# Optimization experiments

Measured on AMD Instinct MI355X. Metric: run time of the kernel, lower is better.

The kernel has to match this reference:

```python
import jax, jax.numpy as jnp
import numpy as np

G, NPG, HID, NLAYERS, MAXZ, K = 256, 128, 256, 3, 1000, 30
N = G * NPG          # 32768 nodes
E = N * 16           # 524288 edges
TOTAL_DIM = HID * NLAYERS + 1  # 769


def setup_inputs():
    key = jax.random.key(0)
    ks = jax.random.split(key, 12)
    z = jax.random.randint(ks[0], (N,), 0, MAXZ)
    edge_index = jax.random.randint(ks[1], (2, E), 0, N)
    batch = jnp.arange(N) // NPG  # contiguous equal-size graphs
    emb = jax.random.normal(ks[2], (MAXZ, HID), jnp.float32)
    s = 1.0 / np.sqrt(HID)
    gcn_w = jax.random.normal(ks[3], (NLAYERS, HID, HID), jnp.float32) * s
    gcn_b = jnp.zeros((NLAYERS, HID), jnp.float32)
    gcn_w_last = jax.random.normal(ks[4], (HID, 1), jnp.float32) * s
    gcn_b_last = jnp.zeros((1,), jnp.float32)
    conv1_w = jax.random.normal(ks[5], (16, 1, 5), jnp.float32) * (1.0 / np.sqrt(5))
    conv1_b = jnp.zeros((16,), jnp.float32)
    conv2_w = jax.random.normal(ks[6], (32, 16, 5), jnp.float32) * (1.0 / np.sqrt(80))
    conv2_b = jnp.zeros((32,), jnp.float32)
    kd = K * TOTAL_DIM            # 23070
    flat = 32 * ((kd - 4) // 2 - 4)  # 368928
    lin1_w = jax.random.normal(ks[7], (128, flat), jnp.float32) * (1.0 / np.sqrt(flat))
    lin1_b = jnp.zeros((128,), jnp.float32)
    lin2_w = jax.random.normal(ks[8], (1, 128), jnp.float32) * (1.0 / np.sqrt(128))
    lin2_b = jnp.zeros((1,), jnp.float32)
    return dict(z=z, edge_index=edge_index, batch=batch, emb=emb, gcn_w=gcn_w,
                gcn_b=gcn_b, gcn_w_last=gcn_w_last, gcn_b_last=gcn_b_last,
                conv1_w=conv1_w, conv1_b=conv1_b, conv2_w=conv2_w, conv2_b=conv2_b,
                lin1_w=lin1_w, lin1_b=lin1_b, lin2_w=lin2_w, lin2_b=lin2_b)


def reference(z, edge_index, batch, emb, gcn_w, gcn_b, gcn_w_last, gcn_b_last,
              conv1_w, conv1_b, conv2_w, conv2_b, lin1_w, lin1_b, lin2_w, lin2_b):
    src, dst = edge_index[0], edge_index[1]
    # GCNConv normalization with self-loops: D^{-1/2}(A+I)D^{-1/2}
    deg = 1.0 + jax.ops.segment_sum(jnp.ones((E,), jnp.float32), dst, num_segments=N)
    dinv = jax.lax.rsqrt(deg)
    enorm = dinv[src] * dinv[dst]   # per-edge norm
    snorm = 1.0 / deg               # self-loop norm

    def gcn(x, W, b):
        xw = x @ W
        agg = jax.ops.segment_sum(enorm[:, None] * xw[src], dst, num_segments=N)
        return agg + snorm[:, None] * xw + b

    x = emb[z]
    xs = []
    for i in range(NLAYERS):
        x = jnp.tanh(gcn(x, gcn_w[i], gcn_b[i]))
        xs.append(x)
    xs.append(jnp.tanh(gcn(x, gcn_w_last, gcn_b_last)))
    h = jnp.concatenate(xs, axis=-1)  # [N, TOTAL_DIM]

    # global_sort_pool: per-graph descending sort by last channel, keep top-k
    hg = h.reshape(G, NPG, TOTAL_DIM)
    order = jnp.argsort(-hg[:, :, -1], axis=1)
    hg = jnp.take_along_axis(hg, order[:, :, None], axis=1)[:, :K]
    p = hg.reshape(G, 1, K * TOTAL_DIM)

    dn = ('NCH', 'OIH', 'NCH')
    c = jax.lax.conv_general_dilated(p, conv1_w, (1,), 'VALID', dimension_numbers=dn)
    c = jax.nn.relu(c + conv1_b[None, :, None])
    c = jax.lax.reduce_window(c, -jnp.inf, jax.lax.max, (1, 1, 2), (1, 1, 2), 'VALID')
    c = jax.lax.conv_general_dilated(c, conv2_w, (1,), 'VALID', dimension_numbers=dn)
    c = jax.nn.relu(c + conv2_b[None, :, None])
    f = c.reshape(G, -1)
    f = jax.nn.relu(f @ lin1_w.T + lin1_b)
    return (f @ lin2_w.T + lin2_b).reshape(-1)
```

## Files before the change

kernel.cpp:

```cpp
#include <hip/hip_runtime.h>

#define NN      32768
#define EE      524288
#define GG      256
#define NPG     128
#define HID     256
#define KTOP    30
#define TD      769
#define HSTR    772
#define PLEN    23070
#define C1LEN   23066
#define POOLLEN 11533
#define C2LEN   11529
#define FLAT    368928
#define L1_KRANGE 512
#define L1_KS   721

#define SWZ(c) ((c) + 4 * ((c) >> 5))

__global__ __launch_bounds__(256) void k_deg(const int* __restrict__ dst, int* __restrict__ deg_cnt) {
    int e = blockIdx.x * 256 + threadIdx.x;
    atomicAdd(&deg_cnt[dst[e]], 1);
}

__global__ __launch_bounds__(256) void k_norm(const int* __restrict__ deg_cnt,
                                              float* __restrict__ dinv, float* __restrict__ snorm) {
    int n = blockIdx.x * 256 + threadIdx.x;
    float dg = 1.0f + (float)deg_cnt[n];
    dinv[n] = rsqrtf(dg);
    snorm[n] = 1.0f / dg;
}

__global__ __launch_bounds__(1024) void k_scan(const int* __restrict__ deg_cnt, int* __restrict__ row_start) {
    __shared__ int sA[1024];
    int t = threadIdx.x;
    int base = t * 32;
    int s = 0;
    for (int i = 0; i < 32; i++) s += deg_cnt[base + i];
    sA[t] = s;
    __syncthreads();
    for (int off = 1; off < 1024; off <<= 1) {
        int v = (t >= off) ? sA[t - off] : 0;
        __syncthreads();
        sA[t] += v;
        __syncthreads();
    }
    int run = sA[t] - s;
    for (int i = 0; i < 32; i++) { row_start[base + i] = run; run += deg_cnt[base + i]; }
}

__global__ __launch_bounds__(256) void k_csrfill(const int* __restrict__ src, const int* __restrict__ dst,
                                                 const int* __restrict__ row_start, int* __restrict__ fill,
                                                 const float* __restrict__ dinv,
                                                 int* __restrict__ csr_src, float* __restrict__ csr_w) {
    int e = blockIdx.x * 256 + threadIdx.x;
    int s = src[e], d = dst[e];
    int pos = row_start[d] + atomicAdd(&fill[d], 1);
    csr_src[pos] = s;
    csr_w[pos] = dinv[s] * dinv[d];
}

__global__ __launch_bounds__(256) void k_embed(const int* __restrict__ z, const float* __restrict__ emb,
                                               float* __restrict__ x) {
    int i = blockIdx.x * 256 + threadIdx.x;
    int n = i >> 6, l = i & 63;
    ((float4*)x)[(size_t)n * 64 + l] = ((const float4*)emb)[(size_t)z[n] * 64 + l];
}

__global__ __launch_bounds__(256) void k_gemm_gcn(const float* __restrict__ A, const float* __restrict__ B,
                                                  float* __restrict__ C) {
    __shared__ float As[16][132];
    __shared__ float Bs[16][140];
    int m0 = blockIdx.x * 128;
    int n0 = blockIdx.y * 128;
    int tid = threadIdx.x;
    int ty = tid >> 4, tx = tid & 15;
    float acc[8][8] = {};
    for (int k0 = 0; k0 < 256; k0 += 16) {
        {
            int m = tid >> 2, kq = (tid & 3) * 4;
            #pragma unroll
            for (int r = 0; r < 2; r++) {
                float4 v = *(const float4*)&A[(size_t)(m0 + m + 64 * r) * 256 + k0 + kq];
                As[kq + 0][m + 64 * r] = v.x;
                As[kq + 1][m + 64 * r] = v.y;
                As[kq + 2][m + 64 * r] = v.z;
                As[kq + 3][m + 64 * r] = v.w;
            }
            int n = (tid & 31) * 4, kk = tid >> 5;
            #pragma unroll
            for (int r = 0; r < 2; r++) {
                float4 v = *(const float4*)&B[(size_t)(k0 + kk + 8 * r) * 256 + n0 + n];
                *(float4*)&Bs[kk + 8 * r][SWZ(n)] = v;
            }
        }
        __syncthreads();
        #pragma unroll
        for (int k = 0; k < 16; k++) {
            float a[8], b[8];
            *(float4*)&a[0] = *(float4*)&As[k][ty * 8];
            *(float4*)&a[4] = *(float4*)&As[k][ty * 8 + 4];
            *(float4*)&b[0] = *(float4*)&Bs[k][SWZ(tx * 8)];
            *(float4*)&b[4] = *(float4*)&Bs[k][SWZ(tx * 8 + 4)];
            #pragma unroll
            for (int i = 0; i < 8; i++)
                #pragma unroll
                for (int j = 0; j < 8; j++) acc[i][j] += a[i] * b[j];
        }
        __syncthreads();
    }
    #pragma unroll
    for (int i = 0; i < 8; i++) {
        int m = m0 + ty * 8 + i;
        float4 v0 = make_float4(acc[i][0], acc[i][1], acc[i][2], acc[i][3]);
        float4 v1 = make_float4(acc[i][4], acc[i][5], acc[i][6], acc[i][7]);
        *(float4*)&C[(size_t)m * 256 + n0 + tx * 8] = v0;
        *(float4*)&C[(size_t)m * 256 + n0 + tx * 8 + 4] = v1;
    }
}

__global__ __launch_bounds__(256) void k_agg(const float* __restrict__ xw, const int* __restrict__ row_start,
                                             const int* __restrict__ deg_cnt, const int* __restrict__ csr_src,
                                             const float* __restrict__ csr_w, const float* __restrict__ snorm,
                                             const float* __restrict__ bias, float* __restrict__ xn,
                                             float* __restrict__ h, int hoff,
                                             const float* __restrict__ wl, float* __restrict__ xwl) {
    int d = blockIdx.x * 4 + (threadIdx.x >> 6);
    int l = threadIdx.x & 63;
    float4 v = ((const float4*)xw)[(size_t)d * 64 + l];
    float sn = snorm[d];
    float4 acc = make_float4(sn * v.x, sn * v.y, sn * v.z, sn * v.w);
    int st = row_start[d], cnt = deg_cnt[d];
    for (int j = 0; j < cnt; j++) {
        int s = csr_src[st + j];
        float w = csr_w[st + j];
        float4 u = ((const float4*)xw)[(size_t)s * 64 + l];
        acc.x += w * u.x; acc.y += w * u.y; acc.z += w * u.z; acc.w += w * u.w;
    }
    float4 b = ((const float4*)bias)[l];
    acc.x = tanhf(acc.x + b.x);
    acc.y = tanhf(acc.y + b.y);
    acc.z = tanhf(acc.z + b.z);
    acc.w = tanhf(acc.w + b.w);
    ((float4*)xn)[(size_t)d * 64 + l] = acc;
    *(float4*)&h[(size_t)d * HSTR + hoff + l * 4] = acc;
    if (wl != nullptr) {
        float4 w4 = ((const float4*)wl)[l];
        float s = acc.x * w4.x + acc.y * w4.y + acc.z * w4.z + acc.w * w4.w;
        #pragma unroll
        for (int off = 32; off; off >>= 1) s += __shfl_down(s, off, 64);
        if (l == 0) xwl[d] = s;
    }
}

__global__ __launch_bounds__(256) void k_agg_last(const float* __restrict__ xwl, const int* __restrict__ row_start,
                                                  const int* __restrict__ deg_cnt, const int* __restrict__ csr_src,
                                                  const float* __restrict__ csr_w, const float* __restrict__ snorm,
                                                  const float* __restrict__ blast, float* __restrict__ h) {
    int d = blockIdx.x * 256 + threadIdx.x;
    float acc = snorm[d] * xwl[d];
    int st = row_start[d], cnt = deg_cnt[d];
    for (int j = 0; j < cnt; j++) acc += csr_w[st + j] * xwl[csr_src[st + j]];
    h[(size_t)d * HSTR + 768] = tanhf(acc + blast[0]);
}

__global__ __launch_bounds__(128) void k_sort_gather(const float* __restrict__ h, float* __restrict__ P) {
    __shared__ float kk[128];
    __shared__ int ii[128];
    int g = blockIdx.x, t = threadIdx.x;
    kk[t] = h[(size_t)(g * 128 + t) * HSTR + 768];
    ii[t] = t;
    __syncthreads();
    for (int size = 2; size <= 128; size <<= 1) {
        for (int stride = size >> 1; stride > 0; stride >>= 1) {
            int p = t ^ stride;
            if (p > t) {
                float ka = kk[t], kbv = kk[p];
                int ia = ii[t], ib = ii[p];
                bool aFirst = (ka > kbv) || (ka == kbv && ia < ib);
                bool asc = (t & size) == 0;
                if (asc != aFirst) { kk[t] = kbv; kk[p] = ka; ii[t] = ib; ii[p] = ia; }
            }
            __syncthreads();
        }
    }
    float* Pg = P + (size_t)g * PLEN;
    for (int r = 0; r < KTOP; r++) {
        const float* srcp = h + (size_t)(g * 128 + ii[r]) * HSTR;
        for (int c = t; c < TD; c += 128) Pg[(size_t)r * TD + c] = srcp[c];
    }
}

#define JT 128
__global__ __launch_bounds__(256) void k_conv(const float* __restrict__ P,
                                              const float* __restrict__ w1, const float* __restrict__ b1,
                                              const float* __restrict__ w2, const float* __restrict__ b2,
                                              float* __restrict__ f) {
    __shared__ float sle[136];
    __shared__ float slo[136];
    __shared__ float pool[16][136];
    __shared__ float w2t[80][32];
    __shared__ float w1s[16][5];
    __shared__ float b1s[16];
    __shared__ float b2s[32];
    int g = blockIdx.x;
    int j0 = blockIdx.y * JT;
    int tid = threadIdx.x;
    const float* Pg = P + (size_t)g * PLEN;
    for (int i = tid; i < 268; i += 256) {
        float v = Pg[min(2 * j0 + i, PLEN - 1)];
        if (i & 1) slo[i >> 1] = v; else sle[i >> 1] = v;
    }
    for (int i = tid; i < 80; i += 256) w1s[i / 5][i % 5] = w1[i];
    if (tid < 16) b1s[tid] = b1[tid];
    if (tid < 32) b2s[tid] = b2[tid];
    for (int i = tid; i < 2560; i += 256) {
        int c2 = i / 80, rem = i % 80;
        w2t[rem][c2] = w2[i];
    }
    __syncthreads();
    for (int i = tid; i < 16 * 132; i += 256) {
        int c1 = i / 132, t = i % 132;
        float e0 = sle[t], o0 = slo[t], e1 = sle[t + 1], o1 = slo[t + 1], e2 = sle[t + 2], o2 = slo[t + 2];
        float w0 = w1s[c1][0], w1v = w1s[c1][1], w2v = w1s[c1][2], w3 = w1s[c1][3], w4 = w1s[c1][4];
        float a = b1s[c1] + w0 * e0 + w1v * o0 + w2v * e1 + w3 * o1 + w4 * e2;
        float b = b1s[c1] + w0 * o0 + w1v * e1 + w2v * o1 + w3 * e2 + w4 * o2;
        pool[c1][t] = fmaxf(fmaxf(a, b), 0.0f);
    }
    __syncthreads();
    int wv = tid >> 6;
    int jl = tid & 63;
    int c2o = wv * 8;
    float acc[8][2];
    #pragma unroll
    for (int cc = 0; cc < 8; cc++) {
        float bb = b2s[c2o + cc];
        acc[cc][0] = bb; acc[cc][1] = bb;
    }
    #pragma unroll 4
    for (int c1 = 0; c1 < 16; c1++) {
        #pragma unroll
        for (int k = 0; k < 5; k++) {
            float4 w0 = *(float4*)&w2t[c1 * 5 + k][c2o];
            float4 w1v = *(float4*)&w2t[c1 * 5 + k][c2o + 4];
            float p0 = pool[c1][jl + k];
            float p1 = pool[c1][jl + 64 + k];
            acc[0][0] += w0.x * p0; acc[0][1] += w0.x * p1;
            acc[1][0] += w0.y * p0; acc[1][1] += w0.y * p1;
            acc[2][0] += w0.z * p0; acc[2][1] += w0.z * p1;
            acc[3][0] += w0.w * p0; acc[3][1] += w0.w * p1;
            acc[4][0] += w1v.x * p0; acc[4][1] += w1v.x * p1;
            acc[5][0] += w1v.y * p0; acc[5][1] += w1v.y * p1;
            acc[6][0] += w1v.z * p0; acc[6][1] += w1v.z * p1;
            acc[7][0] += w1v.w * p0; acc[7][1] += w1v.w * p1;
        }
    }
    size_t fg = (size_t)g * FLAT;
    #pragma unroll
    for (int cc = 0; cc < 8; cc++) {
        #pragma unroll
        for (int jj = 0; jj < 2; jj++) {
            int j = j0 + jl + 64 * jj;
            if (j < C2LEN) f[fg + (size_t)(c2o + cc) * C2LEN + j] = fmaxf(acc[cc][jj], 0.0f);
        }
    }
}

__global__ __launch_bounds__(256) void k_lin1(const float* __restrict__ f, const float* __restrict__ W,
                                              float* __restrict__ partial) {
    __shared__ float As[16][132];
    __shared__ float Bs[16][140];
    int m0 = blockIdx.x * 128;
    int ks = blockIdx.y;
    int kbase = ks * L1_KRANGE;
    int kend = min(kbase + L1_KRANGE, FLAT);
    int tid = threadIdx.x;
    int ty = tid >> 4, tx = tid & 15;
    float acc[8][8] = {};
    for (int k0 = kbase; k0 < kend; k0 += 16) {
        {
            int m = tid >> 2, kq = (tid & 3) * 4;
            #pragma unroll
            for (int r = 0; r < 2; r++) {
                float4 v = *(const float4*)&f[(size_t)(m0 + m + 64 * r) * FLAT + k0 + kq];
                As[kq + 0][m + 64 * r] = v.x;
                As[kq + 1][m + 64 * r] = v.y;
                As[kq + 2][m + 64 * r] = v.z;
                As[kq + 3][m + 64 * r] = v.w;
            }
            int n = tid >> 1, kq2 = (tid & 1) * 8;
            int swn = SWZ(n);
            #pragma unroll
            for (int r = 0; r < 2; r++) {
                int k = kq2 + r * 4;
                float4 v = *(const float4*)&W[(size_t)n * FLAT + k0 + k];
                Bs[k + 0][swn] = v.x; Bs[k + 1][swn] = v.y; Bs[k + 2][swn] = v.z; Bs[k + 3][swn] = v.w;
            }
        }
        __syncthreads();
        #pragma unroll
        for (int k = 0; k < 16; k++) {
            float a[8], b[8];
            *(float4*)&a[0] = *(float4*)&As[k][ty * 8];
            *(float4*)&a[4] = *(float4*)&As[k][ty * 8 + 4];
            *(float4*)&b[0] = *(float4*)&Bs[k][SWZ(tx * 8)];
            *(float4*)&b[4] = *(float4*)&Bs[k][SWZ(tx * 8 + 4)];
            #pragma unroll
            for (int i = 0; i < 8; i++)
                #pragma unroll
                for (int j = 0; j < 8; j++) acc[i][j] += a[i] * b[j];
        }
        __syncthreads();
    }
    #pragma unroll
    for (int i = 0; i < 8; i++) {
        int m = m0 + ty * 8 + i;
        float4 v0 = make_float4(acc[i][0], acc[i][1], acc[i][2], acc[i][3]);
        float4 v1 = make_float4(acc[i][4], acc[i][5], acc[i][6], acc[i][7]);
        *(float4*)&partial[((size_t)ks * 256 + m) * 128 + tx * 8] = v0;
        *(float4*)&partial[((size_t)ks * 256 + m) * 128 + tx * 8 + 4] = v1;
    }
}

__global__ __launch_bounds__(128) void k_reduce(const float* __restrict__ partial, const float* __restrict__ lb1,
                                                const float* __restrict__ lw2, const float* __restrict__ lb2,
                                                float* __restrict__ out) {
    int g = blockIdx.x, o = threadIdx.x;
    float s0 = 0.0f, s1 = 0.0f, s2 = 0.0f, s3 = 0.0f;
    int ks = 0;
    for (; ks + 4 <= L1_KS; ks += 4) {
        s0 += partial[((size_t)(ks + 0) * 256 + g) * 128 + o];
        s1 += partial[((size_t)(ks + 1) * 256 + g) * 128 + o];
        s2 += partial[((size_t)(ks + 2) * 256 + g) * 128 + o];
        s3 += partial[((size_t)(ks + 3) * 256 + g) * 128 + o];
    }
    for (; ks < L1_KS; ks++) s0 += partial[((size_t)ks * 256 + g) * 128 + o];
    float s = (s0 + s1) + (s2 + s3);
    float v = fmaxf(s + lb1[o], 0.0f) * lw2[o];
    #pragma unroll
    for (int off = 32; off; off >>= 1) v += __shfl_down(v, off, 64);
    __shared__ float red[2];
    if ((threadIdx.x & 63) == 0) red[threadIdx.x >> 6] = v;
    __syncthreads();
    if (threadIdx.x == 0) out[g] = red[0] + red[1] + lb2[0];
}

extern "C" void kernel_launch(void* const* d_in, const int* in_sizes, int n_in,
                              void* d_out, int out_size, void* d_ws, size_t ws_size,
                              hipStream_t stream) {
    const int*   z     = (const int*)d_in[0];
    const int*   ei    = (const int*)d_in[1];
    const int*   srcv  = ei;
    const int*   dstv  = ei + EE;
    const float* emb   = (const float*)d_in[3];
    const float* gcnw  = (const float*)d_in[4];
    const float* gcnb  = (const float*)d_in[5];
    const float* wlast = (const float*)d_in[6];
    const float* blast = (const float*)d_in[7];
    const float* w1    = (const float*)d_in[8];
    const float* b1    = (const float*)d_in[9];
    const float* w2    = (const float*)d_in[10];
    const float* b2    = (const float*)d_in[11];
    const float* l1w   = (const float*)d_in[12];
    const float* l1b   = (const float*)d_in[13];
    const float* l2w   = (const float*)d_in[14];
    const float* l2b   = (const float*)d_in[15];
    float* out = (float*)d_out;

    char* base = (char*)d_ws;
    const size_t FB = ((size_t)GG * FLAT * 4 + 511) & ~(size_t)511;
    float* fbuf = (float*)base;
    char* p = base;
    auto alloc = [&](size_t bytes) { void* r = (void*)p; p += (bytes + 511) & ~(size_t)511; return r; };
    int*   deg_cnt = (int*)  alloc((size_t)NN * 4);
    int*   fill    = (int*)  alloc((size_t)NN * 4);
    int*   rowst   = (int*)  alloc((size_t)NN * 4);
    int*   csr_src = (int*)  alloc((size_t)EE * 4);
    float* csr_w   = (float*)alloc((size_t)EE * 4);
    float* dinv    = (float*)alloc((size_t)NN * 4);
    float* snorm   = (float*)alloc((size_t)NN * 4);
    float* xA      = (float*)alloc((size_t)NN * 256 * 4);
    float* xB      = (float*)alloc((size_t)NN * 256 * 4);
    float* xw      = (float*)alloc((size_t)NN * 256 * 4);
    float* h       = (float*)alloc((size_t)NN * HSTR * 4);
    float* xwl     = (float*)alloc((size_t)NN * 4);
    float* P       = (float*)(base + FB);
    float* partial = (float*)(base + FB + (((size_t)GG * PLEN * 4 + 511) & ~(size_t)511));
    (void)ws_size; (void)in_sizes; (void)n_in; (void)out_size;

    hipMemsetAsync(deg_cnt, 0, (size_t)NN * 4, stream);
    hipMemsetAsync(fill,    0, (size_t)NN * 4, stream);

    k_deg    <<<EE / 256, 256, 0, stream>>>(dstv, deg_cnt);
    k_norm   <<<NN / 256, 256, 0, stream>>>(deg_cnt, dinv, snorm);
    k_scan   <<<1, 1024, 0, stream>>>(deg_cnt, rowst);
    k_csrfill<<<EE / 256, 256, 0, stream>>>(srcv, dstv, rowst, fill, dinv, csr_src, csr_w);
    k_embed  <<<NN * 64 / 256, 256, 0, stream>>>(z, emb, xA);

    float* xc = xA;
    float* xn = xB;
    for (int layer = 0; layer < 3; layer++) {
        k_gemm_gcn<<<dim3(NN / 128, 2), 256, 0, stream>>>(xc, gcnw + (size_t)layer * 65536, xw);
        const float* wl = (layer == 2) ? wlast : nullptr;
        k_agg<<<NN / 4, 256, 0, stream>>>(xw, rowst, deg_cnt, csr_src, csr_w, snorm,
                                          gcnb + layer * 256, xn, h, layer * 256, wl, xwl);
        float* t = xc; xc = xn; xn = t;
    }
    k_agg_last<<<NN / 256, 256, 0, stream>>>(xwl, rowst, deg_cnt, csr_src, csr_w, snorm, blast, h);

    k_sort_gather<<<GG, 128, 0, stream>>>(h, P);

    k_conv<<<dim3(GG, (C2LEN + JT - 1) / JT), 256, 0, stream>>>(P, w1, b1, w2, b2, fbuf);

    k_lin1  <<<dim3(2, L1_KS), 256, 0, stream>>>(fbuf, l1w, partial);
    k_reduce<<<GG, 128, 0, stream>>>(partial, l1b, l2w, l2b, out);
}
```

Before: 1.492 ms.

## Restructure conv kernel: persistent tiles, register-blocked conv2, coalesced staged stores

```diff
diff --git a/kernel.cpp b/kernel.cpp
--- a/kernel.cpp
+++ b/kernel.cpp
@@ -65,6 +65,11 @@
     int i = blockIdx.x * 256 + threadIdx.x;
     int n = i >> 6, l = i & 63;
     ((float4*)x)[(size_t)n * 64 + l] = ((const float4*)emb)[(size_t)z[n] * 64 + l];
+}
+
+__global__ __launch_bounds__(256) void k_w2t(const float* __restrict__ w2, float* __restrict__ w2t_g) {
+    for (int i = threadIdx.x; i < 2560; i += 256)
+        w2t_g[i] = w2[(i & 31) * 80 + (i >> 5)];
 }
 
 __global__ __launch_bounds__(256) void k_gemm_gcn(const float* __restrict__ A, const float* __restrict__ B,
@@ -192,76 +197,76 @@
 }
 
 #define JT 128
+#define CONV_T 4
 __global__ __launch_bounds__(256) void k_conv(const float* __restrict__ P,
                                               const float* __restrict__ w1, const float* __restrict__ b1,
-                                              const float* __restrict__ w2, const float* __restrict__ b2,
+                                              const float* __restrict__ w2t_g, const float* __restrict__ b2,
                                               float* __restrict__ f) {
     __shared__ float sle[136];
     __shared__ float slo[136];
     __shared__ float pool[16][136];
-    __shared__ float w2t[80][32];
+    __shared__ float w2t[80][33];
+    __shared__ float outs[32][133];
     __shared__ float w1s[16][5];
     __shared__ float b1s[16];
     __shared__ float b2s[32];
     int g = blockIdx.x;
-    int j0 = blockIdx.y * JT;
     int tid = threadIdx.x;
     const float* Pg = P + (size_t)g * PLEN;
-    for (int i = tid; i < 268; i += 256) {
-        float v = Pg[min(2 * j0 + i, PLEN - 1)];
-        if (i & 1) slo[i >> 1] = v; else sle[i >> 1] = v;
-    }
+    for (int i = tid; i < 2560; i += 256) w2t[i >> 5][i & 31] = w2t_g[i];
     for (int i = tid; i < 80; i += 256) w1s[i / 5][i % 5] = w1[i];
     if (tid < 16) b1s[tid] = b1[tid];
     if (tid < 32) b2s[tid] = b2[tid];
-    for (int i = tid; i < 2560; i += 256) {
-        int c2 = i / 80, rem = i % 80;
-        w2t[rem][c2] = w2[i];
-    }
-    __syncthreads();
-    for (int i = tid; i < 16 * 132; i += 256) {
-        int c1 = i / 132, t = i % 132;
-        float e0 = sle[t], o0 = slo[t], e1 = sle[t + 1], o1 = slo[t + 1], e2 = sle[t + 2], o2 = slo[t + 2];
-        float w0 = w1s[c1][0], w1v = w1s[c1][1], w2v = w1s[c1][2], w3 = w1s[c1][3], w4 = w1s[c1][4];
-        float a = b1s[c1] + w0 * e0 + w1v * o0 + w2v * e1 + w3 * o1 + w4 * e2;
-        float b = b1s[c1] + w0 * o0 + w1v * e1 + w2v * o1 + w3 * e2 + w4 * o2;
-        pool[c1][t] = fmaxf(fmaxf(a, b), 0.0f);
-    }
-    __syncthreads();
-    int wv = tid >> 6;
-    int jl = tid & 63;
-    int c2o = wv * 8;
-    float acc[8][2];
-    #pragma unroll
-    for (int cc = 0; cc < 8; cc++) {
-        float bb = b2s[c2o + cc];
-        acc[cc][0] = bb; acc[cc][1] = bb;
-    }
-    #pragma unroll 4
-    for (int c1 = 0; c1 < 16; c1++) {
+
+    int c2 = tid & 31;
+    int jg = tid >> 5;
+    size_t fg = (size_t)g * FLAT;
+
+    for (int tt = 0; tt < CONV_T; tt++) {
+        int j0 = (blockIdx.y * CONV_T + tt) * JT;
+        if (j0 >= C2LEN) break;
+        __syncthreads();
+        for (int i = tid; i < 268; i += 256) {
+            float v = Pg[min(2 * j0 + i, PLEN - 1)];
+            if (i & 1) slo[i >> 1] = v; else sle[i >> 1] = v;
+        }
+        __syncthreads();
+        for (int i = tid; i < 16 * 132; i += 256) {
+            int c1 = i / 132, t = i % 132;
+            float e0 = sle[t], o0 = slo[t], e1 = sle[t + 1], o1 = slo[t + 1], e2 = sle[t + 2], o2 = slo[t + 2];
+            float u0 = w1s[c1][0], u1 = w1s[c1][1], u2 = w1s[c1][2], u3 = w1s[c1][3], u4 = w1s[c1][4];
+            float a = b1s[c1] + u0 * e0 + u1 * o0 + u2 * e1 + u3 * o1 + u4 * e2;
+            float b = b1s[c1] + u0 * o0 + u1 * e1 + u2 * o1 + u3 * e2 + u4 * o2;
+            pool[c1][t] = fmaxf(fmaxf(a, b), 0.0f);
+        }
+        __syncthreads();
+        float acc[16];
+        float bb = b2s[c2];
         #pragma unroll
-        for (int k = 0; k < 5; k++) {
-            float4 w0 = *(float4*)&w2t[c1 * 5 + k][c2o];
-            float4 w1v = *(float4*)&w2t[c1 * 5 + k][c2o + 4];
-            float p0 = pool[c1][jl + k];
-            float p1 = pool[c1][jl + 64 + k];
-            acc[0][0] += w0.x * p0; acc[0][1] += w0.x * p1;
-            acc[1][0] += w0.y * p0; acc[1][1] += w0.y * p1;
-            acc[2][0] += w0.z * p0; acc[2][1] += w0.z * p1;
-            acc[3][0] += w0.w * p0; acc[3][1] += w0.w * p1;
-            acc[4][0] += w1v.x * p0; acc[4][1] += w1v.x * p1;
-            acc[5][0] += w1v.y * p0; acc[5][1] += w1v.y * p1;
-            acc[6][0] += w1v.z * p0; acc[6][1] += w1v.z * p1;
-            acc[7][0] += w1v.w * p0; acc[7][1] += w1v.w * p1;
-        }
-    }
-    size_t fg = (size_t)g * FLAT;
-    #pragma unroll
-    for (int cc = 0; cc < 8; cc++) {
+        for (int jj = 0; jj < 16; jj++) acc[jj] = bb;
+        int jbase = jg * 16;
+        for (int c1 = 0; c1 < 16; c1++) {
+            float p[20];
+            #pragma unroll
+            for (int q = 0; q < 5; q++) {
+                float4 v = *(float4*)&pool[c1][jbase + q * 4];
+                p[q * 4 + 0] = v.x; p[q * 4 + 1] = v.y; p[q * 4 + 2] = v.z; p[q * 4 + 3] = v.w;
+            }
+            float wk[5];
+            #pragma unroll
+            for (int k = 0; k < 5; k++) wk[k] = w2t[c1 * 5 + k][c2];
+            #pragma unroll
+            for (int k = 0; k < 5; k++)
+                #pragma unroll
+                for (int jj = 0; jj < 16; jj++) acc[jj] += wk[k] * p[jj + k];
+        }
         #pragma unroll
-        for (int jj = 0; jj < 2; jj++) {
-            int j = j0 + jl + 64 * jj;
-            if (j < C2LEN) f[fg + (size_t)(c2o + cc) * C2LEN + j] = fmaxf(acc[cc][jj], 0.0f);
+        for (int jj = 0; jj < 16; jj++) outs[c2][jbase + jj] = fmaxf(acc[jj], 0.0f);
+        __syncthreads();
+        for (int it = 0; it < 16; it++) {
+            int i = tid + it * 256;
+            int cc = i >> 7, j = (i & 127) + j0;
+            if (j < C2LEN) f[fg + (size_t)cc * C2LEN + j] = outs[cc][i & 127];
         }
     }
 }
@@ -386,6 +391,7 @@
     float* xwl     = (float*)alloc((size_t)NN * 4);
     float* P       = (float*)(base + FB);
     float* partial = (float*)(base + FB + (((size_t)GG * PLEN * 4 + 511) & ~(size_t)511));
+    float* w2t_g   = partial + (size_t)L1_KS * 256 * 128;
     (void)ws_size; (void)in_sizes; (void)n_in; (void)out_size;
 
     hipMemsetAsync(deg_cnt, 0, (size_t)NN * 4, stream);
@@ -396,6 +402,7 @@
     k_scan   <<<1, 1024, 0, stream>>>(deg_cnt, rowst);
     k_csrfill<<<EE / 256, 256, 0, stream>>>(srcv, dstv, rowst, fill, dinv, csr_src, csr_w);
     k_embed  <<<NN * 64 / 256, 256, 0, stream>>>(z, emb, xA);
+    k_w2t    <<<1, 256, 0, stream>>>(w2, w2t_g);
 
     float* xc = xA;
     float* xn = xB;
@@ -410,7 +417,8 @@
 
     k_sort_gather<<<GG, 128, 0, stream>>>(h, P);
 
-    k_conv<<<dim3(GG, (C2LEN + JT - 1) / JT), 256, 0, stream>>>(P, w1, b1, w2, b2, fbuf);
+    const int ntiles = (C2LEN + JT - 1) / JT;
+    k_conv<<<dim3(GG, (ntiles + CONV_T - 1) / CONV_T), 256, 0, stream>>>(P, w1, b1, w2t_g, b2, fbuf);
 
     k_lin1  <<<dim3(2, L1_KS), 256, 0, stream>>>(fbuf, l1w, partial);
     k_reduce<<<GG, 128, 0, stream>>>(partial, l1b, l2w, l2b, out);
```

Result: no change. 1.472 ms (-1.3%).
